# Performance work log

Measured on AMD Instinct MI355X. Metric: run time of the kernel, lower is better.

Reference implementation:

```python
import jax, jax.numpy as jnp
import numpy as np

N, E, D = 50000, 800000, 128
LN_EPS = 1e-5


def setup_inputs() -> dict:
    key = jax.random.key(0)
    ks = jax.random.split(key, 6)
    return {
        "x": jax.random.normal(ks[0], (N, D), dtype=jnp.float32),
        "edge_index": jax.random.randint(ks[1], (2, E), 0, N, dtype=jnp.int64),
        "edge_weight": jax.random.uniform(ks[2], (E,), dtype=jnp.float32),
        "lin_w": jax.random.normal(ks[3], (D, D), dtype=jnp.float32) * (1.0 / np.sqrt(D)),
        "lin_b": jax.random.normal(ks[4], (D,), dtype=jnp.float32) * 0.02,
        "ln_gamma": jnp.ones((D,), dtype=jnp.float32),
        "ln_beta": jnp.zeros((D,), dtype=jnp.float32),
    }


def reference(x, edge_index, edge_weight, lin_w, lin_b, ln_gamma, ln_beta):
    n = x.shape[0]
    src, dst = edge_index[0], edge_index[1]
    # degree (by dst), symmetric-ish normalization with +1 smoothing
    deg = jax.ops.segment_sum(jnp.ones(dst.shape, x.dtype), dst, num_segments=n)
    dis = jax.lax.rsqrt(deg + 1.0)  # (N,)
    # gather -> scale -> scatter-add
    scale = (edge_weight * dis[src])[:, None]          # (E,1)
    msg = x[src] * scale                               # (E,D)
    agg = jax.ops.segment_sum(msg, dst, num_segments=n)  # (N,D)
    agg = agg * dis[:, None] + x                       # residual
    # dense tail: Linear -> GELU (exact, matches torch F.gelu) -> LayerNorm
    h = jax.nn.gelu(agg @ lin_w.T + lin_b, approximate=False)
    mu = jnp.mean(h, axis=-1, keepdims=True)
    var = jnp.mean(jnp.square(h - mu), axis=-1, keepdims=True)
    return (h - mu) * jax.lax.rsqrt(var + LN_EPS) * ln_gamma + ln_beta
```

## Files before the change

kernel.cpp:

```cpp
#include <hip/hip_runtime.h>
#include <math.h>

#define D 128
#define CAP 48
#define LDS_STRIDE 136
#define CHUNKS 256
#define BLDS 4096

typedef __bf16  bf16x8 __attribute__((ext_vector_type(8)));
typedef float   f32x4  __attribute__((ext_vector_type(4)));

static __device__ __forceinline__ unsigned short f2bf(float f) {
    unsigned int u = __float_as_uint(f);
    u = (u + 0x7fffu + ((u >> 16) & 1u)) >> 16;
    return (unsigned short)u;
}
static __device__ __forceinline__ unsigned int pack2bf(float lo, float hi) {
    return (unsigned int)f2bf(lo) | ((unsigned int)f2bf(hi) << 16);
}
static __device__ __forceinline__ float bflo(unsigned int u) { return __uint_as_float(u << 16); }
static __device__ __forceinline__ float bfhi(unsigned int u) { return __uint_as_float(u & 0xffff0000u); }


__global__ __launch_bounds__(1024) void k_hist(const int* __restrict__ dst,
                                               int* __restrict__ H,
                                               int* __restrict__ bsum,
                                               int e_count, int cs, int nbk) {
    __shared__ int hist[1024];
    int tid = threadIdx.x, c = blockIdx.x;
    for (int b = tid; b < nbk; b += 1024) hist[b] = 0;
    __syncthreads();
    int lo = c * cs, hi = min(lo + cs, e_count);
    for (int i = lo + tid; i < hi; i += 1024) atomicAdd(&hist[dst[i] >> 6], 1);
    __syncthreads();
    for (int b = tid; b < nbk; b += 1024) {
        int v = hist[b];
        H[b * CHUNKS + c] = v;
        if (v) atomicAdd(&bsum[b], v);
    }
}

__global__ __launch_bounds__(1024) void k_scan_bsum2(int* __restrict__ bsum, int nb) {
    int tid = threadIdx.x, lane = tid & 63, wave = tid >> 6;
    int v = (tid < nb) ? bsum[tid] : 0;
    int incl = v;
    #pragma unroll
    for (int off = 1; off < 64; off <<= 1) {
        int t = __shfl_up(incl, off);
        if (lane >= off) incl += t;
    }
    __shared__ int ws[16];
    if (lane == 63) ws[wave] = incl;
    __syncthreads();
    if (tid == 0) {
        int run = 0;
        #pragma unroll
        for (int i = 0; i < 16; ++i) { int t = ws[i]; ws[i] = run; run += t; }
    }
    __syncthreads();
    if (tid < nb) bsum[tid] = incl - v + ws[wave];
}

__global__ __launch_bounds__(256) void k_applyH(int* __restrict__ H,
                                                const int* __restrict__ bsum_excl, int m) {
    int g = blockIdx.x * 256 + threadIdx.x;
    int tid = threadIdx.x, lane = tid & 63, wave = tid >> 6;
    int v = (g < m) ? H[g] : 0;
    int incl = v;
    #pragma unroll
    for (int off = 1; off < 64; off <<= 1) {
        int t = __shfl_up(incl, off);
        if (lane >= off) incl += t;
    }
    __shared__ int ws[4];
    if (lane == 63) ws[wave] = incl;
    __syncthreads();
    int add = bsum_excl[blockIdx.x];
    for (int i = 0; i < wave; ++i) add += ws[i];
    if (g < m) H[g] = incl - v + add;
}

__global__ __launch_bounds__(1024) void k_scatter(const int* __restrict__ src,
                                                  const int* __restrict__ dst,
                                                  const float* __restrict__ ew,
                                                  const int* __restrict__ H,
                                                  unsigned int* __restrict__ rec,
                                                  int e_count, int cs, int nbk) {
    __shared__ int cur[1024];
    int tid = threadIdx.x, c = blockIdx.x;
    for (int b = tid; b < nbk; b += 1024) cur[b] = H[b * CHUNKS + c];
    __syncthreads();
    int lo = c * cs, hi = min(lo + cs, e_count);
    for (int i = lo + tid; i < hi; i += 1024) {
        int d = dst[i];
        int s = src[i];
        unsigned int q = (unsigned int)(ew[i] * 1023.0f + 0.5f);
        unsigned int r = (q << 22) | ((unsigned int)(d & 63) << 16) | (unsigned int)s;
        int pos = atomicAdd(&cur[d >> 6], 1);
        rec[pos] = r;
    }
}

__global__ __launch_bounds__(256) void k_bucket_sort(unsigned int* __restrict__ rec,
                                                     const int* __restrict__ H,
                                                     int* __restrict__ deg,
                                                     int* __restrict__ offs,
                                                     int e_count, int n, int nbk) {
    __shared__ int hist[64], curs[64];
    __shared__ unsigned int srt[BLDS];
    int tid = threadIdx.x, b = blockIdx.x;
    int start = H[b * CHUNKS];
    int end = (b == nbk - 1) ? e_count : H[(b + 1) * CHUNKS];
    int cnt = min(end - start, BLDS);
    if (tid < 64) hist[tid] = 0;
    __syncthreads();
    for (int i = tid; i < cnt; i += 256) atomicAdd(&hist[(rec[start + i] >> 16) & 63], 1);
    __syncthreads();
    if (tid < 64) {
        int dg = hist[tid];
        int incl = dg;
        #pragma unroll
        for (int off = 1; off < 64; off <<= 1) {
            int t = __shfl_up(incl, off);
            if (tid >= off) incl += t;
        }
        int excl = incl - dg;
        curs[tid] = excl;
        int node = b * 64 + tid;
        if (node < n) {
            deg[node] = dg;
            offs[node] = start + excl;
            if (node == n - 1) offs[n] = e_count;
        }
    }
    __syncthreads();
    for (int i = tid; i < cnt; i += 256) {
        unsigned int r = rec[start + i];
        int rank = atomicAdd(&curs[(r >> 16) & 63], 1);
        srt[rank] = r;
    }
    __syncthreads();
    for (int i = tid; i < cnt; i += 256) rec[start + i] = srt[i];
}


__global__ __launch_bounds__(256) void k_cast(const float* __restrict__ x,
                                              const int* __restrict__ deg,
                                              unsigned short* __restrict__ xs,
                                              const float* __restrict__ W,
                                              unsigned short* __restrict__ Wb, int n) {
    int i4 = blockIdx.x * 256 + threadIdx.x;
    int nq = n * (D / 4);
    if (i4 < nq) {
        int node = i4 >> 5;
        float dd = rsqrtf((float)deg[node] + 1.0f);
        float4 v = ((const float4*)x)[i4];
        ushort4 u;
        u.x = f2bf(v.x * dd); u.y = f2bf(v.y * dd);
        u.z = f2bf(v.z * dd); u.w = f2bf(v.w * dd);
        ((ushort4*)xs)[i4] = u;
    } else {
        int j = i4 - nq;
        if (j < (D * D / 4)) {
            float4 v = ((const float4*)W)[j];
            ushort4 u;
            u.x = f2bf(v.x); u.y = f2bf(v.y);
            u.z = f2bf(v.z); u.w = f2bf(v.w);
            ((ushort4*)Wb)[j] = u;
        }
    }
}


__global__ __launch_bounds__(256) void k_gather_csr(const unsigned short* __restrict__ xs,
                                                    const float* __restrict__ x,
                                                    const int* __restrict__ offs,
                                                    const unsigned int* __restrict__ rec,
                                                    unsigned short* __restrict__ aggbf, int n) {
    int node = (int)((blockIdx.x * blockDim.x + threadIdx.x) >> 6);
    int lane = threadIdx.x & 63;
    if (node >= n) return;
    int beg = offs[node], end = offs[node + 1];
    const float wq = 1.0f / 1023.0f;
    float ax = 0.f, ay = 0.f;

    int e = beg;
    for (; e + 3 < end; e += 4) {
        unsigned int r0 = rec[e + 0], r1 = rec[e + 1], r2 = rec[e + 2], r3 = rec[e + 3];
        unsigned int u0 = ((const unsigned int*)(xs + (size_t)(r0 & 0xffffu) * D))[lane];
        unsigned int u1 = ((const unsigned int*)(xs + (size_t)(r1 & 0xffffu) * D))[lane];
        unsigned int u2 = ((const unsigned int*)(xs + (size_t)(r2 & 0xffffu) * D))[lane];
        unsigned int u3 = ((const unsigned int*)(xs + (size_t)(r3 & 0xffffu) * D))[lane];
        float w0 = (float)(r0 >> 22) * wq;
        float w1 = (float)(r1 >> 22) * wq;
        float w2 = (float)(r2 >> 22) * wq;
        float w3 = (float)(r3 >> 22) * wq;
        ax += w0 * bflo(u0); ay += w0 * bfhi(u0);
        ax += w1 * bflo(u1); ay += w1 * bfhi(u1);
        ax += w2 * bflo(u2); ay += w2 * bfhi(u2);
        ax += w3 * bflo(u3); ay += w3 * bfhi(u3);
    }
    for (; e < end; ++e) {
        unsigned int r = rec[e];
        unsigned int u = ((const unsigned int*)(xs + (size_t)(r & 0xffffu) * D))[lane];
        float w = (float)(r >> 22) * wq;
        ax += w * bflo(u); ay += w * bfhi(u);
    }

    float dd = rsqrtf((float)(end - beg) + 1.0f);
    float2 xv = ((const float2*)(x + (size_t)node * D))[lane];
    ((unsigned int*)(aggbf + (size_t)node * D))[lane] = pack2bf(ax * dd + xv.x, ay * dd + xv.y);
}


__global__ __launch_bounds__(1024) void k_tail_bf(const unsigned short* __restrict__ aggbf,
                                                  float* __restrict__ out,
                                                  const unsigned short* __restrict__ Wb,
                                                  const float* __restrict__ bias,
                                                  const float* __restrict__ gamma,
                                                  const float* __restrict__ beta, int n) {
    __shared__ unsigned short Bl[128 * LDS_STRIDE];

    int tid  = threadIdx.x;
    int lane = tid & 63;
    int wave = tid >> 6;
    int n16  = lane & 15;
    int quad = lane >> 4;

    #pragma unroll
    for (int it = 0; it < 2; ++it) {
        int idx = it * 1024 + tid;
        uint4 w4 = ((const uint4*)Wb)[idx];
        int t  = idx >> 4;
        int k8 = (idx & 15) << 3;
        *(uint4*)&Bl[t * LDS_STRIDE + k8] = w4;
    }
    __syncthreads();

    int row0w = blockIdx.x * 256 + wave * 16;
    int arow  = row0w + n16;

    bf16x8 afr[4];
    #pragma unroll
    for (int ko = 0; ko < 4; ++ko)
        afr[ko] = __builtin_bit_cast(bf16x8,
            *(const uint4*)&aggbf[(size_t)arow * D + ko * 32 + quad * 8]);

    f32x4 acc[8];
    #pragma unroll
    for (int nt = 0; nt < 8; ++nt) acc[nt] = (f32x4){0.f, 0.f, 0.f, 0.f};

    #pragma unroll
    for (int nt = 0; nt < 8; ++nt) {
        #pragma unroll
        for (int ko = 0; ko < 4; ++ko) {
            bf16x8 bfr = __builtin_bit_cast(bf16x8,
                *(const uint4*)&Bl[(nt * 16 + n16) * LDS_STRIDE + ko * 32 + quad * 8]);
            acc[nt] = __builtin_amdgcn_mfma_f32_16x16x32_bf16(afr[ko], bfr, acc[nt], 0, 0, 0);
        }
    }

    float bcol[8], gcol[8], betcol[8];
    #pragma unroll
    for (int nt = 0; nt < 8; ++nt) {
        int col = nt * 16 + n16;
        bcol[nt]   = bias[col];
        gcol[nt]   = gamma[col];
        betcol[nt] = beta[col];
    }

    #pragma unroll
    for (int r = 0; r < 4; ++r) {
        float h[8];
        float s1 = 0.f, s2 = 0.f;
        #pragma unroll
        for (int nt = 0; nt < 8; ++nt) {
            float v = acc[nt][r] + bcol[nt];
            v = 0.5f * v * (1.0f + erff(v * 0.70710678118654752f));
            h[nt] = v;
            s1 += v; s2 += v * v;
        }
        #pragma unroll
        for (int mask = 1; mask < 16; mask <<= 1) {
            s1 += __shfl_xor(s1, mask);
            s2 += __shfl_xor(s2, mask);
        }
        float mu  = s1 * (1.0f / 128.0f);
        float var = s2 * (1.0f / 128.0f) - mu * mu;
        float inv = rsqrtf(var + 1e-5f);
        int row = row0w + quad * 4 + r;
        if (row < n) {
            #pragma unroll
            for (int nt = 0; nt < 8; ++nt)
                out[(size_t)row * D + nt * 16 + n16] = (h[nt] - mu) * inv * gcol[nt] + betcol[nt];
        }
    }
}


__global__ __launch_bounds__(256) void k_fillp8(const int* __restrict__ src,
                                                const int* __restrict__ dst,
                                                const float* __restrict__ ew,
                                                int* __restrict__ cnt,
                                                int2* __restrict__ rec, int e_count) {
    int e = blockIdx.x * blockDim.x + threadIdx.x;
    if (e >= e_count) return;
    int d = dst[e];
    int pos = atomicAdd(&cnt[d], 1);
    if (pos < CAP)
        rec[(size_t)d * CAP + pos] = make_int2(src[e], __float_as_int(ew[e]));
}

__global__ __launch_bounds__(256) void k_gatherp_f32(const float* __restrict__ x,
                                                     const int* __restrict__ cnt,
                                                     const int2* __restrict__ rec,
                                                     float* __restrict__ agg, int n) {
    int node = (int)((blockIdx.x * blockDim.x + threadIdx.x) >> 6);
    int lane = threadIdx.x & 63;
    if (node >= n) return;
    int c = cnt[node];
    int m = min(c, CAP);
    size_t base = (size_t)node * CAP;
    float ax = 0.f, ay = 0.f;
    for (int i = 0; i < m; ++i) {
        int2 p = rec[base + i];
        float w = __int_as_float(p.y) * rsqrtf((float)cnt[p.x] + 1.0f);
        float2 v = ((const float2*)(x + (size_t)p.x * D))[lane];
        ax += w * v.x; ay += w * v.y;
    }
    float dd = rsqrtf((float)c + 1.0f);
    float2 xv = ((const float2*)(x + (size_t)node * D))[lane];
    float2 o;
    o.x = ax * dd + xv.x;
    o.y = ay * dd + xv.y;
    ((float2*)(agg + (size_t)node * D))[lane] = o;
}

__global__ __launch_bounds__(256) void k_tail_mfma(float* __restrict__ io,
                                                   const float* __restrict__ W,
                                                   const float* __restrict__ bias,
                                                   const float* __restrict__ gamma,
                                                   const float* __restrict__ beta, int n) {
    __shared__ unsigned short Bl[128 * LDS_STRIDE];
    __shared__ unsigned short Al[4][16 * LDS_STRIDE];

    int tid  = threadIdx.x;
    int lane = tid & 63;
    int wave = tid >> 6;
    int n16  = lane & 15;
    int quad = lane >> 4;

    #pragma unroll
    for (int it = 0; it < 16; ++it) {
        int idx4 = it * 256 + tid;
        float4 w4 = ((const float4*)W)[idx4];
        int t  = idx4 >> 5;
        int k4 = (idx4 & 31) << 2;
        ushort4 u;
        u.x = f2bf(w4.x); u.y = f2bf(w4.y); u.z = f2bf(w4.z); u.w = f2bf(w4.w);
        *(ushort4*)&Bl[t * LDS_STRIDE + k4] = u;
    }
    int row0w = blockIdx.x * 64 + wave * 16;
    #pragma unroll
    for (int j = 0; j < 8; ++j) {
        int idx4 = j * 64 + lane;
        int m  = idx4 >> 5;
        int k4 = (idx4 & 31) << 2;
        int row = row0w + m;
        float4 a4 = make_float4(0.f, 0.f, 0.f, 0.f);
        if (row < n) a4 = ((const float4*)(io + (size_t)row * D))[idx4 & 31];
        ushort4 u;
        u.x = f2bf(a4.x); u.y = f2bf(a4.y); u.z = f2bf(a4.z); u.w = f2bf(a4.w);
        *(ushort4*)&Al[wave][m * LDS_STRIDE + k4] = u;
    }
    __syncthreads();

    bf16x8 afr[4];
    #pragma unroll
    for (int ko = 0; ko < 4; ++ko)
        afr[ko] = __builtin_bit_cast(bf16x8,
            *(const uint4*)&Al[wave][n16 * LDS_STRIDE + ko * 32 + quad * 8]);

    f32x4 acc[8];
    #pragma unroll
    for (int nt = 0; nt < 8; ++nt) acc[nt] = (f32x4){0.f, 0.f, 0.f, 0.f};

    #pragma unroll
    for (int nt = 0; nt < 8; ++nt) {
        #pragma unroll
        for (int ko = 0; ko < 4; ++ko) {
            bf16x8 bfr = __builtin_bit_cast(bf16x8,
                *(const uint4*)&Bl[(nt * 16 + n16) * LDS_STRIDE + ko * 32 + quad * 8]);
            acc[nt] = __builtin_amdgcn_mfma_f32_16x16x32_bf16(afr[ko], bfr, acc[nt], 0, 0, 0);
        }
    }

    float bcol[8], gcol[8], betcol[8];
    #pragma unroll
    for (int nt = 0; nt < 8; ++nt) {
        int col = nt * 16 + n16;
        bcol[nt]   = bias[col];
        gcol[nt]   = gamma[col];
        betcol[nt] = beta[col];
    }

    #pragma unroll
    for (int r = 0; r < 4; ++r) {
        float h[8];
        float s1 = 0.f, s2 = 0.f;
        #pragma unroll
        for (int nt = 0; nt < 8; ++nt) {
            float v = acc[nt][r] + bcol[nt];
            v = 0.5f * v * (1.0f + erff(v * 0.70710678118654752f));
            h[nt] = v;
            s1 += v; s2 += v * v;
        }
        #pragma unroll
        for (int mask = 1; mask < 16; mask <<= 1) {
            s1 += __shfl_xor(s1, mask);
            s2 += __shfl_xor(s2, mask);
        }
        float mu  = s1 * (1.0f / 128.0f);
        float var = s2 * (1.0f / 128.0f) - mu * mu;
        float inv = rsqrtf(var + 1e-5f);
        int row = row0w + quad * 4 + r;
        if (row < n) {
            #pragma unroll
            for (int nt = 0; nt < 8; ++nt)
                io[(size_t)row * D + nt * 16 + n16] = (h[nt] - mu) * inv * gcol[nt] + betcol[nt];
        }
    }
}


extern "C" void kernel_launch(void* const* d_in, const int* in_sizes, int n_in,
                              void* d_out, int out_size, void* d_ws, size_t ws_size,
                              hipStream_t stream) {
    const float* x    = (const float*)d_in[0];
    const int*   ei   = (const int*)d_in[1];
    const float* ew   = (const float*)d_in[2];
    const float* linw = (const float*)d_in[3];
    const float* linb = (const float*)d_in[4];
    const float* lng  = (const float*)d_in[5];
    const float* lnb  = (const float*)d_in[6];
    float* out = (float*)d_out;

    int n = in_sizes[0] / D;
    int e = in_sizes[1] / 2;
    const int* src = ei;
    const int* dst = ei + e;

    int nbk = (n + 63) / 64;
    int m   = nbk * CHUNKS;
    int cs  = (e + CHUNKS - 1) / CHUNKS;
    int gb  = (n + 3) / 4;
    int tb  = (n + 255) / 256;

    char* wsp = (char*)d_ws;
    size_t off = 0;
    auto alloc = [&](size_t bytes) { char* p = wsp + off; off = (off + bytes + 255) & ~(size_t)255; return p; };
    int*            H     = (int*)alloc((size_t)m * 4);
    int*            bsumH = (int*)alloc((size_t)nbk * 4);
    unsigned int*   rec   = (unsigned int*)alloc((size_t)e * 4);
    int*            deg   = (int*)alloc((size_t)n * 4);
    int*            offs  = (int*)alloc((size_t)(n + 1) * 4);
    unsigned short* xs    = (unsigned short*)alloc((size_t)n * D * 2);
    unsigned short* Wb    = (unsigned short*)alloc((size_t)D * D * 2);
    unsigned short* aggbf = (unsigned short*)alloc(((size_t)n + 256) * D * 2);
    bool big = (off <= ws_size) && (n <= 65535) && (nbk <= 1024);

    if (big) {
        hipMemsetAsync(bsumH, 0, (size_t)nbk * 4, stream);
        k_hist<<<CHUNKS, 1024, 0, stream>>>(dst, H, bsumH, e, cs, nbk);
        k_scan_bsum2<<<1, 1024, 0, stream>>>(bsumH, nbk);
        k_applyH<<<nbk, 256, 0, stream>>>(H, bsumH, m);
        k_scatter<<<CHUNKS, 1024, 0, stream>>>(src, dst, ew, H, rec, e, cs, nbk);
        k_bucket_sort<<<nbk, 256, 0, stream>>>(rec, H, deg, offs, e, n, nbk);
        int cb = (n * (D / 4) + (D * D / 4) + 255) / 256;
        k_cast<<<cb, 256, 0, stream>>>(x, deg, xs, linw, Wb, n);
        k_gather_csr<<<gb, 256, 0, stream>>>(xs, x, offs, rec, aggbf, n);
        k_tail_bf<<<tb, 1024, 0, stream>>>(aggbf, out, Wb, linb, lng, lnb, n);
    } else {
        size_t off2 = 0;
        auto alloc2 = [&](size_t bytes) { char* p = wsp + off2; off2 = (off2 + bytes + 255) & ~(size_t)255; return p; };
        int*  cnt2 = (int*)alloc2((size_t)n * 4);
        int2* rec8 = (int2*)alloc2((size_t)n * CAP * 8);
        hipMemsetAsync(cnt2, 0, (size_t)n * 4, stream);
        int eb = (e + 255) / 256;
        int tb64 = (n + 63) / 64;
        k_fillp8<<<eb, 256, 0, stream>>>(src, dst, ew, cnt2, rec8, e);
        k_gatherp_f32<<<gb, 256, 0, stream>>>(x, cnt2, rec8, out, n);
        k_tail_mfma<<<tb64, 256, 0, stream>>>(out, linw, linb, lng, lnb, n);
    }
}
```

Before: 181.4 us.

## Replace scan-based bucket offsets with fixed-capacity buckets and fuse cast into sort

The histogram, two prefix-scan kernels and the separate scatter are replaced by one kernel that reserves space in fixed-capacity per-bucket regions of 2048 slots using global atomic counters. The x-to-bf16 cast is folded into the per-bucket sort kernel, and the weight conversion to bf16 moves into the tail kernel's LDS load. The goal is to cut kernel launches and global passes over the edge arrays. In exchange it relies on no bucket overflowing its capacity, which is only guarded by an average-degree check, and it adds more work per tail block.

```diff
diff --git a/kernel.cpp b/kernel.cpp
--- a/kernel.cpp
+++ b/kernel.cpp
@@ -5,7 +5,8 @@
 #define CAP 48
 #define LDS_STRIDE 136
 #define CHUNKS 256
-#define BLDS 4096
+#define BCAP 2048
+#define BSH 11
 
 typedef __bf16  bf16x8 __attribute__((ext_vector_type(8)));
 typedef float   f32x4  __attribute__((ext_vector_type(4)));
@@ -21,12 +22,14 @@
 static __device__ __forceinline__ float bflo(unsigned int u) { return __uint_as_float(u << 16); }
 static __device__ __forceinline__ float bfhi(unsigned int u) { return __uint_as_float(u & 0xffff0000u); }
 
-
-__global__ __launch_bounds__(1024) void k_hist(const int* __restrict__ dst,
-                                               int* __restrict__ H,
-                                               int* __restrict__ bsum,
-                                               int e_count, int cs, int nbk) {
+__global__ __launch_bounds__(1024) void k_scatter_direct(const int* __restrict__ src,
+                                                         const int* __restrict__ dst,
+                                                         const float* __restrict__ ew,
+                                                         int* __restrict__ gcnt,
+                                                         unsigned int* __restrict__ rec,
+                                                         int e_count, int cs, int nbk) {
     __shared__ int hist[1024];
+    __shared__ int cur[1024];
     int tid = threadIdx.x, c = blockIdx.x;
     for (int b = tid; b < nbk; b += 1024) hist[b] = 0;
     __syncthreads();
@@ -34,87 +37,34 @@
     for (int i = lo + tid; i < hi; i += 1024) atomicAdd(&hist[dst[i] >> 6], 1);
     __syncthreads();
     for (int b = tid; b < nbk; b += 1024) {
-        int v = hist[b];
-        H[b * CHUNKS + c] = v;
-        if (v) atomicAdd(&bsum[b], v);
-    }
-}
-
-__global__ __launch_bounds__(1024) void k_scan_bsum2(int* __restrict__ bsum, int nb) {
-    int tid = threadIdx.x, lane = tid & 63, wave = tid >> 6;
-    int v = (tid < nb) ? bsum[tid] : 0;
-    int incl = v;
-    #pragma unroll
-    for (int off = 1; off < 64; off <<= 1) {
-        int t = __shfl_up(incl, off);
-        if (lane >= off) incl += t;
-    }
-    __shared__ int ws[16];
-    if (lane == 63) ws[wave] = incl;
-    __syncthreads();
-    if (tid == 0) {
-        int run = 0;
-        #pragma unroll
-        for (int i = 0; i < 16; ++i) { int t = ws[i]; ws[i] = run; run += t; }
-    }
-    __syncthreads();
-    if (tid < nb) bsum[tid] = incl - v + ws[wave];
-}
-
-__global__ __launch_bounds__(256) void k_applyH(int* __restrict__ H,
-                                                const int* __restrict__ bsum_excl, int m) {
-    int g = blockIdx.x * 256 + threadIdx.x;
-    int tid = threadIdx.x, lane = tid & 63, wave = tid >> 6;
-    int v = (g < m) ? H[g] : 0;
-    int incl = v;
-    #pragma unroll
-    for (int off = 1; off < 64; off <<= 1) {
-        int t = __shfl_up(incl, off);
-        if (lane >= off) incl += t;
-    }
-    __shared__ int ws[4];
-    if (lane == 63) ws[wave] = incl;
-    __syncthreads();
-    int add = bsum_excl[blockIdx.x];
-    for (int i = 0; i < wave; ++i) add += ws[i];
-    if (g < m) H[g] = incl - v + add;
-}
-
-__global__ __launch_bounds__(1024) void k_scatter(const int* __restrict__ src,
-                                                  const int* __restrict__ dst,
-                                                  const float* __restrict__ ew,
-                                                  const int* __restrict__ H,
-                                                  unsigned int* __restrict__ rec,
-                                                  int e_count, int cs, int nbk) {
-    __shared__ int cur[1024];
-    int tid = threadIdx.x, c = blockIdx.x;
-    for (int b = tid; b < nbk; b += 1024) cur[b] = H[b * CHUNKS + c];
-    __syncthreads();
-    int lo = c * cs, hi = min(lo + cs, e_count);
+        int h = hist[b];
+        int base = h ? atomicAdd(&gcnt[b], h) : 0;
+        cur[b] = (b << BSH) + base;
+    }
+    __syncthreads();
     for (int i = lo + tid; i < hi; i += 1024) {
         int d = dst[i];
-        int s = src[i];
         unsigned int q = (unsigned int)(ew[i] * 1023.0f + 0.5f);
-        unsigned int r = (q << 22) | ((unsigned int)(d & 63) << 16) | (unsigned int)s;
+        unsigned int r = (q << 22) | ((unsigned int)(d & 63) << 16) | (unsigned int)src[i];
         int pos = atomicAdd(&cur[d >> 6], 1);
         rec[pos] = r;
     }
 }
 
-__global__ __launch_bounds__(256) void k_bucket_sort(unsigned int* __restrict__ rec,
-                                                     const int* __restrict__ H,
-                                                     int* __restrict__ deg,
-                                                     int* __restrict__ offs,
-                                                     int e_count, int n, int nbk) {
+__global__ __launch_bounds__(256) void k_sortcast(unsigned int* __restrict__ rec,
+                                                  const int* __restrict__ gcnt,
+                                                  const float* __restrict__ x,
+                                                  unsigned short* __restrict__ xs,
+                                                  int* __restrict__ deg,
+                                                  int* __restrict__ offs, int n) {
     __shared__ int hist[64], curs[64];
-    __shared__ unsigned int srt[BLDS];
+    __shared__ unsigned int srt[BCAP];
     int tid = threadIdx.x, b = blockIdx.x;
-    int start = H[b * CHUNKS];
-    int end = (b == nbk - 1) ? e_count : H[(b + 1) * CHUNKS];
-    int cnt = min(end - start, BLDS);
+    int base = b << BSH;
+    int cnt = min(gcnt[b], BCAP);
     if (tid < 64) hist[tid] = 0;
     __syncthreads();
-    for (int i = tid; i < cnt; i += 256) atomicAdd(&hist[(rec[start + i] >> 16) & 63], 1);
+    for (int i = tid; i < cnt; i += 256) atomicAdd(&hist[(rec[base + i] >> 16) & 63], 1);
     __syncthreads();
     if (tid < 64) {
         int dg = hist[tid];
@@ -128,45 +78,29 @@
         curs[tid] = excl;
         int node = b * 64 + tid;
         if (node < n) {
-            deg[node] = dg;
-            offs[node] = start + excl;
-            if (node == n - 1) offs[n] = e_count;
+            deg[node]  = dg;
+            offs[node] = base + excl;
         }
     }
     __syncthreads();
     for (int i = tid; i < cnt; i += 256) {
-        unsigned int r = rec[start + i];
+        unsigned int r = rec[base + i];
         int rank = atomicAdd(&curs[(r >> 16) & 63], 1);
         srt[rank] = r;
     }
     __syncthreads();
-    for (int i = tid; i < cnt; i += 256) rec[start + i] = srt[i];
-}
-
-
-__global__ __launch_bounds__(256) void k_cast(const float* __restrict__ x,
-                                              const int* __restrict__ deg,
-                                              unsigned short* __restrict__ xs,
-                                              const float* __restrict__ W,
-                                              unsigned short* __restrict__ Wb, int n) {
-    int i4 = blockIdx.x * 256 + threadIdx.x;
-    int nq = n * (D / 4);
-    if (i4 < nq) {
-        int node = i4 >> 5;
-        float dd = rsqrtf((float)deg[node] + 1.0f);
-        float4 v = ((const float4*)x)[i4];
-        ushort4 u;
-        u.x = f2bf(v.x * dd); u.y = f2bf(v.y * dd);
-        u.z = f2bf(v.z * dd); u.w = f2bf(v.w * dd);
-        ((ushort4*)xs)[i4] = u;
-    } else {
-        int j = i4 - nq;
-        if (j < (D * D / 4)) {
-            float4 v = ((const float4*)W)[j];
+    for (int i = tid; i < cnt; i += 256) rec[base + i] = srt[i];
+
+    for (int i4 = tid; i4 < 64 * 32; i4 += 256) {
+        int lm   = i4 >> 5;
+        int node = b * 64 + lm;
+        if (node < n) {
+            float dd = rsqrtf((float)hist[lm] + 1.0f);
+            float4 v = ((const float4*)x)[(size_t)node * 32 + (i4 & 31)];
             ushort4 u;
-            u.x = f2bf(v.x); u.y = f2bf(v.y);
-            u.z = f2bf(v.z); u.w = f2bf(v.w);
-            ((ushort4*)Wb)[j] = u;
+            u.x = f2bf(v.x * dd); u.y = f2bf(v.y * dd);
+            u.z = f2bf(v.z * dd); u.w = f2bf(v.w * dd);
+            ((ushort4*)xs)[(size_t)node * 32 + (i4 & 31)] = u;
         }
     }
 }
@@ -175,12 +109,15 @@
 __global__ __launch_bounds__(256) void k_gather_csr(const unsigned short* __restrict__ xs,
                                                     const float* __restrict__ x,
                                                     const int* __restrict__ offs,
+                                                    const int* __restrict__ deg,
                                                     const unsigned int* __restrict__ rec,
                                                     unsigned short* __restrict__ aggbf, int n) {
     int node = (int)((blockIdx.x * blockDim.x + threadIdx.x) >> 6);
     int lane = threadIdx.x & 63;
     if (node >= n) return;
-    int beg = offs[node], end = offs[node + 1];
+    int beg = offs[node];
+    int dgv = deg[node];
+    int end = beg + dgv;
     const float wq = 1.0f / 1023.0f;
     float ax = 0.f, ay = 0.f;
 
@@ -207,7 +144,7 @@
         ax += w * bflo(u); ay += w * bfhi(u);
     }
 
-    float dd = rsqrtf((float)(end - beg) + 1.0f);
+    float dd = rsqrtf((float)dgv + 1.0f);
     float2 xv = ((const float2*)(x + (size_t)node * D))[lane];
     ((unsigned int*)(aggbf + (size_t)node * D))[lane] = pack2bf(ax * dd + xv.x, ay * dd + xv.y);
 }
@@ -215,7 +152,7 @@
 
 __global__ __launch_bounds__(1024) void k_tail_bf(const unsigned short* __restrict__ aggbf,
                                                   float* __restrict__ out,
-                                                  const unsigned short* __restrict__ Wb,
+                                                  const float* __restrict__ W,
                                                   const float* __restrict__ bias,
                                                   const float* __restrict__ gamma,
                                                   const float* __restrict__ beta, int n) {
@@ -228,12 +165,14 @@
     int quad = lane >> 4;
 
     #pragma unroll
-    for (int it = 0; it < 2; ++it) {
-        int idx = it * 1024 + tid;
-        uint4 w4 = ((const uint4*)Wb)[idx];
-        int t  = idx >> 4;
-        int k8 = (idx & 15) << 3;
-        *(uint4*)&Bl[t * LDS_STRIDE + k8] = w4;
+    for (int it = 0; it < 4; ++it) {
+        int idx4 = it * 1024 + tid;
+        float4 w4 = ((const float4*)W)[idx4];
+        int t  = idx4 >> 5;
+        int k4 = (idx4 & 31) << 2;
+        ushort4 u;
+        u.x = f2bf(w4.x); u.y = f2bf(w4.y); u.z = f2bf(w4.z); u.w = f2bf(w4.w);
+        *(ushort4*)&Bl[t * LDS_STRIDE + k4] = u;
     }
     __syncthreads();
 
@@ -451,7 +390,6 @@
     const int* dst = ei + e;
 
     int nbk = (n + 63) / 64;
-    int m   = nbk * CHUNKS;
     int cs  = (e + CHUNKS - 1) / CHUNKS;
     int gb  = (n + 3) / 4;
     int tb  = (n + 255) / 256;
@@ -459,27 +397,21 @@
     char* wsp = (char*)d_ws;
     size_t off = 0;
     auto alloc = [&](size_t bytes) { char* p = wsp + off; off = (off + bytes + 255) & ~(size_t)255; return p; };
-    int*            H     = (int*)alloc((size_t)m * 4);
-    int*            bsumH = (int*)alloc((size_t)nbk * 4);
-    unsigned int*   rec   = (unsigned int*)alloc((size_t)e * 4);
+    int*            gcnt  = (int*)alloc((size_t)nbk * 4);
+    unsigned int*   rec   = (unsigned int*)alloc((size_t)nbk * BCAP * 4);
     int*            deg   = (int*)alloc((size_t)n * 4);
-    int*            offs  = (int*)alloc((size_t)(n + 1) * 4);
+    int*            offs  = (int*)alloc((size_t)n * 4);
     unsigned short* xs    = (unsigned short*)alloc((size_t)n * D * 2);
-    unsigned short* Wb    = (unsigned short*)alloc((size_t)D * D * 2);
     unsigned short* aggbf = (unsigned short*)alloc(((size_t)n + 256) * D * 2);
-    bool big = (off <= ws_size) && (n <= 65535) && (nbk <= 1024);
+    bool big = (off <= ws_size) && (n <= 65535) && (nbk <= 1024)
+               && ((size_t)e <= (size_t)nbk * (BCAP / 2));
 
     if (big) {
-        hipMemsetAsync(bsumH, 0, (size_t)nbk * 4, stream);
-        k_hist<<<CHUNKS, 1024, 0, stream>>>(dst, H, bsumH, e, cs, nbk);
-        k_scan_bsum2<<<1, 1024, 0, stream>>>(bsumH, nbk);
-        k_applyH<<<nbk, 256, 0, stream>>>(H, bsumH, m);
-        k_scatter<<<CHUNKS, 1024, 0, stream>>>(src, dst, ew, H, rec, e, cs, nbk);
-        k_bucket_sort<<<nbk, 256, 0, stream>>>(rec, H, deg, offs, e, n, nbk);
-        int cb = (n * (D / 4) + (D * D / 4) + 255) / 256;
-        k_cast<<<cb, 256, 0, stream>>>(x, deg, xs, linw, Wb, n);
-        k_gather_csr<<<gb, 256, 0, stream>>>(xs, x, offs, rec, aggbf, n);
-        k_tail_bf<<<tb, 1024, 0, stream>>>(aggbf, out, Wb, linb, lng, lnb, n);
+        hipMemsetAsync(gcnt, 0, (size_t)nbk * 4, stream);
+        k_scatter_direct<<<CHUNKS, 1024, 0, stream>>>(src, dst, ew, gcnt, rec, e, cs, nbk);
+        k_sortcast<<<nbk, 256, 0, stream>>>(rec, gcnt, x, xs, deg, offs, n);
+        k_gather_csr<<<gb, 256, 0, stream>>>(xs, x, offs, deg, rec, aggbf, n);
+        k_tail_bf<<<tb, 1024, 0, stream>>>(aggbf, out, linw, linb, lng, lnb, n);
     } else {
         size_t off2 = 0;
         auto alloc2 = [&](size_t bytes) { char* p = wsp + off2; off2 = (off2 + bytes + 255) & ~(size_t)255; return p; };
```

Result: faster. 167.2 us (-7.8%).
